# Kernel optimization log

Hardware: AMD Instinct MI355X
Metric: run time of the kernel (lower is better)

Reference implementation:

```python
import jax, jax.numpy as jnp
import numpy as np

LAT_DIM = 4  # 4D lattice (T, X, Y, Z)


def setup_inputs() -> dict:
    key = jax.random.key(0)
    k1, k2 = jax.random.split(key)
    # field: [batch, T, X, Y, Z, color=3, spin=4]
    field = jax.random.normal(k1, (16, 32, 16, 16, 16, 3, 4), dtype=jnp.float32)
    # gauge_field: [n_dirs=4, T, X, Y, Z, 3, 3]
    gauge_field = jax.random.normal(k2, (4, 32, 16, 16, 16, 3, 3), dtype=jnp.float32)
    return {"field": field, "gauge_field": gauge_field, "direction": 1}


def reference(field, gauge_field, direction):
    # direction is a static Python int (module hyperparameter)
    if direction == 0:
        return field
    s = 1 if direction > 0 else -1
    d = abs(direction)
    # periodic neighbor shift of the fermion field along lattice axis d-1
    # field axis index: d - (3 + LAT_DIM) (negative indexing, skips batch)
    out = jnp.roll(field, shift=s, axis=d - (3 + LAT_DIM))
    gp = gauge_field[d - 1]  # [T,X,Y,Z,3,3]
    if direction > 0:
        # dagger(roll(U)) -> for real matrices dagger == transpose
        gauge = jnp.swapaxes(jnp.roll(gp, shift=s, axis=d - 1), -1, -2)
    else:
        gauge = gp
    # per-site small matmul: [T,X,Y,Z,3,3] @ [B,T,X,Y,Z,3,4] -> [B,T,X,Y,Z,3,4]
    return jnp.matmul(gauge, out)
```

## Files before the change

### kernel.cpp

```cpp
#include <hip/hip_runtime.h>

constexpr int TD = 32, XD = 16, YD = 16, ZD = 16;
constexpr int NSITE  = TD * XD * YD * ZD;
constexpr int NBATCH = 16;
constexpr int BPT    = 2;
constexpr int NGROUP = NBATCH / BPT;

typedef float v4f __attribute__((ext_vector_type(4)));

__global__ __launch_bounds__(256) void qshift_kernel(
    const float* __restrict__ field,
    const float* __restrict__ gauge,
    const int*   __restrict__ dir_p,
    float*       __restrict__ out)
{
    long tid = (long)blockIdx.x * blockDim.x + threadIdx.x;
    if (tid >= (long)NSITE * NGROUP) return;
    const int site = (int)(tid & (NSITE - 1));
    const int bgrp = (int)(tid >> 17);
    const int b0   = bgrp * BPT;
    const int dir  = *dir_p;

    const long fbase_site = (long)b0 * NSITE;

    if (dir == 0) {
        const v4f* src = (const v4f*)field + (fbase_site + site) * 3;
        v4f*       dst = (v4f*)out        + (fbase_site + site) * 3;
        #pragma unroll
        for (int i = 0; i < BPT; ++i) {
            const long off = (long)i * NSITE * 3;
            dst[off + 0] = src[off + 0];
            dst[off + 1] = src[off + 1];
            dst[off + 2] = src[off + 2];
        }
        return;
    }

    const int d = (dir > 0) ? dir : -dir;
    const int a = d - 1;

    const int shift = (a == 0) ? 12 : (a == 1) ? 8 : (a == 2) ? 4 : 0;
    const int len   = (a == 0) ? TD : 16;

    const int ca = (site >> shift) & (len - 1);
    int cs;
    bool transpose;
    if (dir > 0) {
        cs = (ca == 0) ? (len - 1) : (ca - 1);
        transpose = true;
    } else {
        cs = (ca == len - 1) ? 0 : (ca + 1);
        transpose = false;
    }
    const int srcsite = site + ((cs - ca) << shift);
    const int gsite   = (dir > 0) ? srcsite : site;

    const float* gp = gauge + ((long)a * NSITE + (long)gsite) * 9;
    float g0 = gp[0], g1 = gp[1], g2 = gp[2];
    float g3 = gp[3], g4 = gp[4], g5 = gp[5];
    float g6 = gp[6], g7 = gp[7], g8 = gp[8];

    float m00, m01, m02, m10, m11, m12, m20, m21, m22;
    if (transpose) {
        m00 = g0; m01 = g3; m02 = g6;
        m10 = g1; m11 = g4; m12 = g7;
        m20 = g2; m21 = g5; m22 = g8;
    } else {
        m00 = g0; m01 = g1; m02 = g2;
        m10 = g3; m11 = g4; m12 = g5;
        m20 = g6; m21 = g7; m22 = g8;
    }

    const v4f* fsrc = (const v4f*)field + (fbase_site + srcsite) * 3;
    v4f*       dst  = (v4f*)out        + (fbase_site + site) * 3;

    #pragma unroll
    for (int i = 0; i < BPT; ++i) {
        const long off = (long)i * NSITE * 3;
        const v4f f0 = fsrc[off + 0];
        const v4f f1 = fsrc[off + 1];
        const v4f f2 = fsrc[off + 2];
        dst[off + 0] = m00*f0 + m01*f1 + m02*f2;
        dst[off + 1] = m10*f0 + m11*f1 + m12*f2;
        dst[off + 2] = m20*f0 + m21*f1 + m22*f2;
    }
}

extern "C" void kernel_launch(void* const* d_in, const int* in_sizes, int n_in,
                              void* d_out, int out_size, void* d_ws, size_t ws_size,
                              hipStream_t stream) {
    const float* field = (const float*)d_in[0];
    const float* gauge = (const float*)d_in[1];
    const int*   dirp  = (const int*)d_in[2];
    float*       outp  = (float*)d_out;

    const long nthreads = (long)NSITE * NGROUP;
    const int  block = 256;
    const int  grid  = (int)((nthreads + block - 1) / block);
    qshift_kernel<<<grid, block, 0, stream>>>(field, gauge, dirp, outp);
}
```

Measured before the change: 38.08 us.

## Map one thread per color row with LDS-staged neighbor rows

Each thread now owns one 16-byte color row (site*3+c) instead of a whole site, so global loads and stores are fully contiguous across a wavefront. Each wavefront stages the shifted field rows plus a small halo in LDS, and each thread reads its site's three rows from LDS to compute one output row. Each thread loads only its gauge row or column, and it now handles 4 batch entries instead of 2. This adds LDS traffic and halo loads, and relies on there being no barrier because each wave only reads its own LDS region.

```diff
diff --git a/kernel.cpp b/kernel.cpp
--- a/kernel.cpp
+++ b/kernel.cpp
@@ -2,9 +2,11 @@
 
 constexpr int TD = 32, XD = 16, YD = 16, ZD = 16;
 constexpr int NSITE  = TD * XD * YD * ZD;
+constexpr int PLANE  = NSITE * 3;
 constexpr int NBATCH = 16;
-constexpr int BPT    = 2;
+constexpr int BPT    = 4;
 constexpr int NGROUP = NBATCH / BPT;
+constexpr int WPB    = 4;
 
 typedef float v4f __attribute__((ext_vector_type(4)));
 
@@ -14,75 +16,77 @@
     const int*   __restrict__ dir_p,
     float*       __restrict__ out)
 {
-    long tid = (long)blockIdx.x * blockDim.x + threadIdx.x;
-    if (tid >= (long)NSITE * NGROUP) return;
-    const int site = (int)(tid & (NSITE - 1));
-    const int bgrp = (int)(tid >> 17);
-    const int b0   = bgrp * BPT;
+    __shared__ v4f stage[WPB][BPT][68];
+
+    const int lane = threadIdx.x & 63;
+    const int w    = threadIdx.x >> 6;
+    const int jj   = blockIdx.x * 256 + threadIdx.x;
+    const int b0   = blockIdx.y * BPT;
     const int dir  = *dir_p;
 
-    const long fbase_site = (long)b0 * NSITE;
+    const v4f* f4 = (const v4f*)field;
+    v4f*       o4 = (v4f*)out;
 
     if (dir == 0) {
-        const v4f* src = (const v4f*)field + (fbase_site + site) * 3;
-        v4f*       dst = (v4f*)out        + (fbase_site + site) * 3;
         #pragma unroll
-        for (int i = 0; i < BPT; ++i) {
-            const long off = (long)i * NSITE * 3;
-            dst[off + 0] = src[off + 0];
-            dst[off + 1] = src[off + 1];
-            dst[off + 2] = src[off + 2];
+        for (int k = 0; k < BPT; ++k) {
+            const long idx = (long)(b0 + k) * PLANE + jj;
+            o4[idx] = f4[idx];
         }
         return;
     }
 
-    const int d = (dir > 0) ? dir : -dir;
-    const int a = d - 1;
-
+    const int d     = (dir > 0) ? dir : -dir;
+    const int a     = d - 1;
     const int shift = (a == 0) ? 12 : (a == 1) ? 8 : (a == 2) ? 4 : 0;
     const int len   = (a == 0) ? TD : 16;
 
-    const int ca = (site >> shift) & (len - 1);
-    int cs;
-    bool transpose;
-    if (dir > 0) {
-        cs = (ca == 0) ? (len - 1) : (ca - 1);
-        transpose = true;
-    } else {
-        cs = (ca == len - 1) ? 0 : (ca + 1);
-        transpose = false;
-    }
-    const int srcsite = site + ((cs - ca) << shift);
-    const int gsite   = (dir > 0) ? srcsite : site;
+    auto srcidx = [&](int j) -> int {
+        const int s  = (int)((unsigned)j / 3u);
+        const int cc = j - s * 3;
+        const int ca = (s >> shift) & (len - 1);
+        const int cs = (dir > 0) ? ((ca == 0) ? (len - 1) : (ca - 1))
+                                 : ((ca == len - 1) ? 0 : (ca + 1));
+        return (s + ((cs - ca) << shift)) * 3 + cc;
+    };
 
+    const int site = (int)((unsigned)jj / 3u);
+    const int c    = jj - site * 3;
+    const int ca   = (site >> shift) & (len - 1);
+    const int cs   = (dir > 0) ? ((ca == 0) ? (len - 1) : (ca - 1))
+                               : ((ca == len - 1) ? 0 : (ca + 1));
+    const int ssite   = site + ((cs - ca) << shift);
+    const int src_own = ssite * 3 + c;
+
+    const int gsite = (dir > 0) ? ssite : site;
     const float* gp = gauge + ((long)a * NSITE + (long)gsite) * 9;
-    float g0 = gp[0], g1 = gp[1], g2 = gp[2];
-    float g3 = gp[3], g4 = gp[4], g5 = gp[5];
-    float g6 = gp[6], g7 = gp[7], g8 = gp[8];
+    float m0, m1, m2;
+    if (dir > 0) { m0 = gp[c];     m1 = gp[3 + c];   m2 = gp[6 + c];   }
+    else         { m0 = gp[3 * c]; m1 = gp[3 * c + 1]; m2 = gp[3 * c + 2]; }
 
-    float m00, m01, m02, m10, m11, m12, m20, m21, m22;
-    if (transpose) {
-        m00 = g0; m01 = g3; m02 = g6;
-        m10 = g1; m11 = g4; m12 = g7;
-        m20 = g2; m21 = g5; m22 = g8;
-    } else {
-        m00 = g0; m01 = g1; m02 = g2;
-        m10 = g3; m11 = g4; m12 = g5;
-        m20 = g6; m21 = g7; m22 = g8;
+    int halo_slot = 0, src_halo = 0;
+    if (lane < 4) {
+        const int joff = (lane < 2) ? (lane - 2) : (62 + lane);
+        int jh = (jj - lane) + joff;
+        jh = (jh < 0) ? 0 : ((jh >= PLANE) ? (PLANE - 1) : jh);
+        halo_slot = (lane < 2) ? lane : (lane + 64);
+        src_halo  = srcidx(jh);
     }
 
-    const v4f* fsrc = (const v4f*)field + (fbase_site + srcsite) * 3;
-    v4f*       dst  = (v4f*)out        + (fbase_site + site) * 3;
+    #pragma unroll
+    for (int k = 0; k < BPT; ++k) {
+        const long pb = (long)(b0 + k) * PLANE;
+        stage[w][k][2 + lane] = f4[pb + src_own];
+        if (lane < 4) stage[w][k][halo_slot] = f4[pb + src_halo];
+    }
 
+    const int p = lane + 2 - c;
     #pragma unroll
-    for (int i = 0; i < BPT; ++i) {
-        const long off = (long)i * NSITE * 3;
-        const v4f f0 = fsrc[off + 0];
-        const v4f f1 = fsrc[off + 1];
-        const v4f f2 = fsrc[off + 2];
-        dst[off + 0] = m00*f0 + m01*f1 + m02*f2;
-        dst[off + 1] = m10*f0 + m11*f1 + m12*f2;
-        dst[off + 2] = m20*f0 + m21*f1 + m22*f2;
+    for (int k = 0; k < BPT; ++k) {
+        const v4f f0 = stage[w][k][p];
+        const v4f f1 = stage[w][k][p + 1];
+        const v4f f2 = stage[w][k][p + 2];
+        o4[(long)(b0 + k) * PLANE + jj] = m0 * f0 + m1 * f1 + m2 * f2;
     }
 }
 
@@ -94,8 +98,6 @@
     const int*   dirp  = (const int*)d_in[2];
     float*       outp  = (float*)d_out;
 
-    const long nthreads = (long)NSITE * NGROUP;
-    const int  block = 256;
-    const int  grid  = (int)((nthreads + block - 1) / block);
-    qshift_kernel<<<grid, block, 0, stream>>>(field, gauge, dirp, outp);
+    dim3 grid(PLANE / 256, NGROUP);
+    qshift_kernel<<<grid, 256, 0, stream>>>(field, gauge, dirp, outp);
 }
```

New measurement: 39.15 us. +2.8%, slower.
